# Optimization experiments

Measured on AMD Instinct MI355X. Metric: run time of the kernel, lower is better.

## Reference

```python
import jax, jax.numpy as jnp
import numpy as np


def setup_inputs() -> dict:
    key = jax.random.key(0)
    k1, k2 = jax.random.split(key)
    B, N, M, D = 8, 4096, 4096, 3
    pred_points = jax.random.normal(k1, (B, N, D), dtype=jnp.float32)
    gt_points = jax.random.normal(k2, (B, M, D), dtype=jnp.float32)
    return {"pred_points": pred_points, "gt_points": gt_points}


def _chamfer_l2(pred, gt):
    # pytorch3d chamfer_distance with norm=2 uses SQUARED euclidean distances.
    x2 = jnp.sum(pred * pred, axis=-1)            # [B, N]
    y2 = jnp.sum(gt * gt, axis=-1)                # [B, M]
    xy = jnp.einsum('bnd,bmd->bnm', pred, gt)     # [B, N, M]
    d = x2[:, :, None] + y2[:, None, :] - 2.0 * xy
    d = jnp.maximum(d, 0.0)  # numerical safety
    cham_x = jnp.mean(jnp.min(d, axis=2), axis=1)  # mean over N, per batch
    cham_y = jnp.mean(jnp.min(d, axis=1), axis=1)  # mean over M, per batch
    # batch_reduction='mean', loss = cham_x + cham_y
    return jnp.mean(cham_x) + jnp.mean(cham_y)


def reference(pred_points, gt_points):
    return _chamfer_l2(pred_points.astype(jnp.float32), gt_points.astype(jnp.float32))
```

## Files before the change

### kernel.cpp

```cpp
#include <hip/hip_runtime.h>


#define CH_NPTS   4096
#define CH_HALF   32768
#define CH_NQ     65536
#define CH_C      8
#define CH_TGT    512
#define CH_GROUPS 128

typedef float f32x2 __attribute__((ext_vector_type(2)));
typedef float f32x4 __attribute__((ext_vector_type(4)));


__global__ __launch_bounds__(256) void chamfer_pack(
    const float* __restrict__ pred, const float* __restrict__ gt,
    float* __restrict__ X, float* __restrict__ Y,
    float* __restrict__ Z, float* __restrict__ W,
    float* __restrict__ out)
{
    const int i = blockIdx.x * 256 + threadIdx.x;
    if (i == 0) out[0] = 0.0f;
    const int p = i & (CH_HALF - 1);
    const float* src = (i >> 15) ? gt : pred;
    const float x = src[p * 3 + 0];
    const float y = src[p * 3 + 1];
    const float z = src[p * 3 + 2];
    X[i] = x; Y[i] = y; Z[i] = z;
    W[i] = fmaf(x, x, fmaf(y, y, z * z));
}

__global__ __launch_bounds__(256) void chamfer_main(
    const float* __restrict__ X, const float* __restrict__ Y,
    const float* __restrict__ Z, const float* __restrict__ W,
    float* __restrict__ partial)
{
    const int tid   = threadIdx.x;
    const int group = blockIdx.x >> 3;
    const int chunk = blockIdx.x & 7;
    const int dir   = group >> 6;
    const int b     = (group >> 3) & 7;

    const int qa = group * 512 + tid;
    const int qb = qa + 256;
    f32x2 axx, ayy, azz, bxx, byy, bzz;
    axx[0] = axx[1] = -2.f * X[qa];
    ayy[0] = ayy[1] = -2.f * Y[qa];
    azz[0] = azz[1] = -2.f * Z[qa];
    bxx[0] = bxx[1] = -2.f * X[qb];
    byy[0] = byy[1] = -2.f * Y[qb];
    bzz[0] = bzz[1] = -2.f * Z[qb];

    const int toff = (dir ^ 1) * CH_HALF + b * CH_NPTS + chunk * CH_TGT;
    const f32x4* __restrict__ X4 = (const f32x4*)(X + toff);
    const f32x4* __restrict__ Y4 = (const f32x4*)(Y + toff);
    const f32x4* __restrict__ Z4 = (const f32x4*)(Z + toff);
    const f32x4* __restrict__ W4 = (const f32x4*)(W + toff);

    const float INF = 3.4028235e38f;
    float mA0 = INF, mA1 = INF, mB0 = INF, mB1 = INF;

    #pragma unroll 2
    for (int j = 0; j < CH_TGT / 4; ++j) {
        const f32x4 Xs = X4[j];
        const f32x4 Ys = Y4[j];
        const f32x4 Zs = Z4[j];
        const f32x4 Ws = W4[j];

        #pragma unroll
        for (int h = 0; h < 2; ++h) {
            f32x2 xs, ys, zs, wv;
            xs[0] = Xs[2 * h]; xs[1] = Xs[2 * h + 1];
            ys[0] = Ys[2 * h]; ys[1] = Ys[2 * h + 1];
            zs[0] = Zs[2 * h]; zs[1] = Zs[2 * h + 1];
            wv[0] = Ws[2 * h]; wv[1] = Ws[2 * h + 1];

            const f32x2 ea = __builtin_elementwise_fma(
                xs, axx, __builtin_elementwise_fma(
                    ys, ayy, __builtin_elementwise_fma(zs, azz, wv)));
            const f32x2 eb = __builtin_elementwise_fma(
                xs, bxx, __builtin_elementwise_fma(
                    ys, byy, __builtin_elementwise_fma(zs, bzz, wv)));

            if (h) {
                mA1 = fminf(fminf(mA1, ea[0]), ea[1]);
                mB1 = fminf(fminf(mB1, eb[0]), eb[1]);
            } else {
                mA0 = fminf(fminf(mA0, ea[0]), ea[1]);
                mB0 = fminf(fminf(mB0, eb[0]), eb[1]);
            }
        }
    }

    partial[chunk * CH_NQ + qa] = fminf(mA0, mA1);
    partial[chunk * CH_NQ + qb] = fminf(mB0, mB1);
}

__global__ __launch_bounds__(256) void chamfer_reduce(
    const float* __restrict__ W, const float* __restrict__ partial,
    float* __restrict__ out)
{
    __shared__ float wsum[4];
    const int i = blockIdx.x * 256 + threadIdx.x;

    float m = partial[i];
    #pragma unroll
    for (int c = 1; c < CH_C; ++c)
        m = fminf(m, partial[c * CH_NQ + i]);
    const float d = fmaxf(W[i] + m, 0.0f);

    float s = d * (1.0f / (8.0f * 4096.0f));
    #pragma unroll
    for (int off = 32; off > 0; off >>= 1)
        s += __shfl_down(s, off);

    if ((threadIdx.x & 63) == 0) wsum[threadIdx.x >> 6] = s;
    __syncthreads();
    if (threadIdx.x == 0)
        atomicAdd(out, wsum[0] + wsum[1] + wsum[2] + wsum[3]);
}

extern "C" void kernel_launch(void* const* d_in, const int* in_sizes, int n_in,
                              void* d_out, int out_size, void* d_ws, size_t ws_size,
                              hipStream_t stream) {
    const float* pred = (const float*)d_in[0];
    const float* gt   = (const float*)d_in[1];
    float* out        = (float*)d_out;

    float* X       = (float*)d_ws;
    float* Y       = X + CH_NQ;
    float* Z       = Y + CH_NQ;
    float* W       = Z + CH_NQ;
    float* partial = W + CH_NQ;

    chamfer_pack  <<<CH_NQ / 256, 256, 0, stream>>>(pred, gt, X, Y, Z, W, out);
    chamfer_main  <<<CH_GROUPS * CH_C, 256, 0, stream>>>(X, Y, Z, W, partial);
    chamfer_reduce<<<CH_NQ / 256, 256, 0, stream>>>(W, partial, out);
}
```

Measured before the change: 85.79 us.

## Stage target tiles in LDS and split targets into more chunks

The main kernel now copies its target tile (x, y, z, |p|^2) into shared memory once per block and reads it from LDS inside the inner loop, where before every thread made uniform global loads. The chunk count doubles to 16 and the tile size halves to 256, giving twice as many blocks with shorter loops. The reduce kernel still runs its min loop over CH_C, so it now reads 16 partials per point, which adds partial-buffer traffic. Launch bounds now ask for 8 blocks per CU.

```diff
diff --git a/kernel.cpp b/kernel.cpp
--- a/kernel.cpp
+++ b/kernel.cpp
@@ -4,8 +4,8 @@
 #define CH_NPTS   4096
 #define CH_HALF   32768
 #define CH_NQ     65536
-#define CH_C      8
-#define CH_TGT    512
+#define CH_C      16
+#define CH_TGT    256
 #define CH_GROUPS 128
 
 typedef float f32x2 __attribute__((ext_vector_type(2)));
@@ -29,42 +29,51 @@
     W[i] = fmaf(x, x, fmaf(y, y, z * z));
 }
 
-__global__ __launch_bounds__(256) void chamfer_main(
-    const float* __restrict__ X, const float* __restrict__ Y,
-    const float* __restrict__ Z, const float* __restrict__ W,
-    float* __restrict__ partial)
+__global__ __launch_bounds__(256, 8) void chamfer_main(
+    const float* __restrict__ X, float* __restrict__ partial)
 {
+    __shared__ alignas(16) float sT[4][CH_TGT];
+
     const int tid   = threadIdx.x;
-    const int group = blockIdx.x >> 3;
-    const int chunk = blockIdx.x & 7;
+    const int group = blockIdx.x >> 4;
+    const int chunk = blockIdx.x & 15;
     const int dir   = group >> 6;
     const int b     = (group >> 3) & 7;
+
+    const int toff = (dir ^ 1) * CH_HALF + b * CH_NPTS + chunk * CH_TGT;
+    {
+        const int arr = tid >> 6;
+        const int idx = tid & 63;
+        reinterpret_cast<float4*>(sT)[tid] =
+            reinterpret_cast<const float4*>(X + arr * CH_NQ + toff)[idx];
+    }
 
     const int qa = group * 512 + tid;
     const int qb = qa + 256;
     f32x2 axx, ayy, azz, bxx, byy, bzz;
     axx[0] = axx[1] = -2.f * X[qa];
-    ayy[0] = ayy[1] = -2.f * Y[qa];
-    azz[0] = azz[1] = -2.f * Z[qa];
+    ayy[0] = ayy[1] = -2.f * X[CH_NQ + qa];
+    azz[0] = azz[1] = -2.f * X[2 * CH_NQ + qa];
     bxx[0] = bxx[1] = -2.f * X[qb];
-    byy[0] = byy[1] = -2.f * Y[qb];
-    bzz[0] = bzz[1] = -2.f * Z[qb];
+    byy[0] = byy[1] = -2.f * X[CH_NQ + qb];
+    bzz[0] = bzz[1] = -2.f * X[2 * CH_NQ + qb];
 
-    const int toff = (dir ^ 1) * CH_HALF + b * CH_NPTS + chunk * CH_TGT;
-    const f32x4* __restrict__ X4 = (const f32x4*)(X + toff);
-    const f32x4* __restrict__ Y4 = (const f32x4*)(Y + toff);
-    const f32x4* __restrict__ Z4 = (const f32x4*)(Z + toff);
-    const f32x4* __restrict__ W4 = (const f32x4*)(W + toff);
+    __syncthreads();
+
+    const f32x4* __restrict__ Xl = reinterpret_cast<const f32x4*>(&sT[0][0]);
+    const f32x4* __restrict__ Yl = reinterpret_cast<const f32x4*>(&sT[1][0]);
+    const f32x4* __restrict__ Zl = reinterpret_cast<const f32x4*>(&sT[2][0]);
+    const f32x4* __restrict__ Wl = reinterpret_cast<const f32x4*>(&sT[3][0]);
 
     const float INF = 3.4028235e38f;
     float mA0 = INF, mA1 = INF, mB0 = INF, mB1 = INF;
 
     #pragma unroll 2
     for (int j = 0; j < CH_TGT / 4; ++j) {
-        const f32x4 Xs = X4[j];
-        const f32x4 Ys = Y4[j];
-        const f32x4 Zs = Z4[j];
-        const f32x4 Ws = W4[j];
+        const f32x4 Xs = Xl[j];
+        const f32x4 Ys = Yl[j];
+        const f32x4 Zs = Zl[j];
+        const f32x4 Ws = Wl[j];
 
         #pragma unroll
         for (int h = 0; h < 2; ++h) {
@@ -133,6 +142,6 @@
     float* partial = W + CH_NQ;
 
     chamfer_pack  <<<CH_NQ / 256, 256, 0, stream>>>(pred, gt, X, Y, Z, W, out);
-    chamfer_main  <<<CH_GROUPS * CH_C, 256, 0, stream>>>(X, Y, Z, W, partial);
+    chamfer_main  <<<CH_GROUPS * CH_C, 256, 0, stream>>>(X, partial);
     chamfer_reduce<<<CH_NQ / 256, 256, 0, stream>>>(W, partial, out);
 }
```

Measured after the change: 84.14 us. About the same (-1.9%).
